# Kernel tuning notes

Hardware: AMD Instinct MI355X
Metric: run time of the kernel (lower is better)

Reference implementation:

```python
import jax, jax.numpy as jnp
import numpy as np

B, C, D, H, W = 2, 32, 96, 96, 96
RED = 16
INV_SQRT2 = 0.7071067811865476  # 1/sqrt(2), Haar analysis filter coefficient
BN_EPS = 1e-5


def _haar1(x, axis):
    # pywt 'haar' DWT on even-length signals: a[i]=(x[2i]+x[2i+1])/sqrt2, d[i]=(x[2i]-x[2i+1])/sqrt2
    e = jax.lax.slice_in_dim(x, 0, None, stride=2, axis=axis)
    o = jax.lax.slice_in_dim(x, 1, None, stride=2, axis=axis)
    return (e + o) * INV_SQRT2, (e - o) * INV_SQRT2


def haar_dwt3d(x):
    # x: (B, C, D, H, W). Separable 3D Haar DWT; key letters follow pywt dwtn
    # axis order (D, H, W): 'aad' = approx along D, approx along H, detail along W.
    aD, dD = _haar1(x, 2)
    aa, ad = _haar1(aD, 3)
    da, dd = _haar1(dD, 3)
    aaa, aad = _haar1(aa, 4)
    ada, add = _haar1(ad, 4)
    daa, dad = _haar1(da, 4)
    dda, ddd = _haar1(dd, 4)
    # per-channel grouping of 7 detail bands, then flatten to (B, 7C, D/2, H/2, W/2)
    high = jnp.stack([aad, ada, add, daa, dad, dda, ddd], axis=2)
    b, c = x.shape[0], x.shape[1]
    high = high.reshape(b, c * 7, *aaa.shape[2:])
    return aaa, high


def chan_attn(x, w1, w2):
    # AdaptiveAvgPool3d(1) -> FC(no bias) -> ReLU -> FC(no bias) -> Sigmoid -> scale
    y = x.mean(axis=(2, 3, 4))                     # (B, Ch)
    y = jax.nn.sigmoid(jnp.maximum(y @ w1.T, 0.0) @ w2.T)
    return x * y[:, :, None, None, None]


def setup_inputs() -> dict:
    key = jax.random.key(0)
    ks = jax.random.split(key, 7)
    x = jax.random.normal(ks[0], (B, C, D, H, W), dtype=jnp.float32)
    w1_low = jax.random.normal(ks[1], (C // RED, C), dtype=jnp.float32) * 0.1
    w2_low = jax.random.normal(ks[2], (C, C // RED), dtype=jnp.float32) * 0.1
    w1_high = jax.random.normal(ks[3], (7 * C // RED, 7 * C), dtype=jnp.float32) * 0.05
    w2_high = jax.random.normal(ks[4], (7 * C, 7 * C // RED), dtype=jnp.float32) * 0.05
    w_fuse = jax.random.normal(ks[5], (C, 8 * C), dtype=jnp.float32) * 0.05  # 1x1x1 conv kernel
    b_fuse = jnp.zeros((C,), dtype=jnp.float32)
    gamma = jnp.ones((C,), dtype=jnp.float32)
    beta = jnp.zeros((C,), dtype=jnp.float32)
    return dict(x=x, w1_low=w1_low, w2_low=w2_low, w1_high=w1_high, w2_high=w2_high,
                w_fuse=w_fuse, b_fuse=b_fuse, gamma=gamma, beta=beta)


def reference(x, w1_low, w2_low, w1_high, w2_high, w_fuse, b_fuse, gamma, beta):
    low, high = haar_dwt3d(x)                                  # (B,C,48,48,48), (B,7C,48,48,48)
    low = chan_attn(low, w1_low, w2_low)
    high = chan_attn(high, w1_high, w2_high)
    z = jnp.concatenate([low, high], axis=1)                   # (B, 8C, 48,48,48)
    z = jnp.einsum('bcdhw,oc->bodhw', z, w_fuse) + b_fuse[None, :, None, None, None]
    # BatchNorm3d (training-mode batch statistics, as fresh torch module defaults)
    mu = z.mean(axis=(0, 2, 3, 4), keepdims=True)
    var = z.var(axis=(0, 2, 3, 4), keepdims=True)
    z = (z - mu) * jax.lax.rsqrt(var + BN_EPS)
    z = z * gamma[None, :, None, None, None] + beta[None, :, None, None, None]
    return jnp.maximum(z, 0.0)
```

## Files before the change

kernel.cpp:

```cpp
#include <hip/hip_runtime.h>
#include <math.h>

#define HS 0.35355339059327373f
#define NSPAT 110592
#define NBN   221184

__global__ __launch_bounds__(256) void k1_parity(const float* __restrict__ x,
                                                 float* __restrict__ S) {
    int blk = blockIdx.x;
    int d   = blk % 96;
    int bc  = blk / 96;
    const float4* x4 = (const float4*)x + (long)blk * 2304;
    int tid = threadIdx.x;
    float aE0 = 0.f, aO0 = 0.f, aE1 = 0.f, aO1 = 0.f;
#pragma unroll
    for (int i = 0; i < 9; ++i) {
        int f = tid + i * 256;
        float4 v = x4[f];
        int h = f / 24;
        float e = v.x + v.z, o = v.y + v.w;
        if (h & 1) { aE1 += e; aO1 += o; }
        else       { aE0 += e; aO0 += o; }
    }
#pragma unroll
    for (int m = 32; m; m >>= 1) {
        aE0 += __shfl_xor(aE0, m, 64); aO0 += __shfl_xor(aO0, m, 64);
        aE1 += __shfl_xor(aE1, m, 64); aO1 += __shfl_xor(aO1, m, 64);
    }
    __shared__ float red[4][4];
    int lane = tid & 63, wave = tid >> 6;
    if (lane == 0) { red[wave][0] = aE0; red[wave][1] = aO0;
                     red[wave][2] = aE1; red[wave][3] = aO1; }
    __syncthreads();
    if (tid < 4) {
        float v = red[0][tid] + red[1][tid] + red[2][tid] + red[3][tid];
        int q = tid >> 1, r = tid & 1, p = d & 1;
        atomicAdd(&S[bc * 8 + p * 4 + q * 2 + r], v);
    }
}

__global__ __launch_bounds__(256) void k2_attn(
        const float* __restrict__ S,
        const float* __restrict__ w1l, const float* __restrict__ w2l,
        const float* __restrict__ w1h, const float* __restrict__ w2h,
        const float* __restrict__ wf, float* __restrict__ A) {
    int b = blockIdx.x, tid = threadIdx.x;
    __shared__ float mlow[32], mhigh[224], h1l[2], h1h[14], ylow[32], yhigh[224];
    const float* Sb = S + b * 256;
    const float MS = HS / (float)NSPAT;
    if (tid < 32) {
        float s = 0.f;
        for (int j = 0; j < 8; ++j) s += Sb[tid * 8 + j];
        mlow[tid] = s * MS;
    }
    if (tid < 224) {
        int c = tid / 7, k = tid % 7, dm = k + 1;
        float s = 0.f;
        for (int j = 0; j < 8; ++j) {
            float sg = (__popc(j & dm) & 1) ? -1.f : 1.f;
            s += sg * Sb[c * 8 + j];
        }
        mhigh[tid] = s * MS;
    }
    __syncthreads();
    if (tid < 2) {
        float s = 0.f;
        for (int c = 0; c < 32; ++c) s += w1l[tid * 32 + c] * mlow[c];
        h1l[tid] = fmaxf(s, 0.f);
    } else if (tid < 16) {
        int j = tid - 2;
        float s = 0.f;
        for (int c = 0; c < 224; ++c) s += w1h[j * 224 + c] * mhigh[c];
        h1h[j] = fmaxf(s, 0.f);
    }
    __syncthreads();
    if (tid < 32) {
        float s = w2l[tid * 2] * h1l[0] + w2l[tid * 2 + 1] * h1l[1];
        ylow[tid] = 1.f / (1.f + expf(-s));
    } else if (tid < 256) {
        int i = tid - 32;
        float s = 0.f;
        for (int j = 0; j < 14; ++j) s += w2h[i * 14 + j] * h1h[j];
        yhigh[i] = 1.f / (1.f + expf(-s));
    }
    __syncthreads();
    for (int idx = tid; idx < 8192; idx += 256) {
        int o = idx >> 8, c = (idx >> 3) & 31, pqr = idx & 7;
        float a = wf[o * 256 + c] * ylow[c];
#pragma unroll
        for (int k = 0; k < 7; ++k) {
            float sg = (__popc(pqr & (k + 1)) & 1) ? -1.f : 1.f;
            a += sg * wf[o * 256 + 32 + c * 7 + k] * yhigh[c * 7 + k];
        }
        A[b * 8192 + idx] = a * HS;
    }
}

__global__ __launch_bounds__(192) void k3_main(const float* __restrict__ x,
                                               const float* __restrict__ A,
                                               float* __restrict__ z,
                                               float* __restrict__ bnSum,
                                               float* __restrict__ bnSq) {
    __shared__ float ldsA[4096];
    __shared__ float red[3][32];
    int blk = blockIdx.x;
    int og  = blk & 1;
    int tmp = blk >> 1;
    int ohg = tmp % 6;
    tmp /= 6;
    int od  = tmp % 48;
    int b   = tmp / 48;
    int tid = threadIdx.x;
    const float* Ab = A + b * 8192 + og * 4096;
    for (int i = tid; i < 4096; i += 192) ldsA[i] = Ab[i];
    __syncthreads();

    int row = tid / 24;
    int t   = tid % 24;
    int oh  = ohg * 8 + row;

    float acc0[16], acc1[16];
#pragma unroll
    for (int o = 0; o < 16; ++o) { acc0[o] = 0.f; acc1[o] = 0.f; }

    const float4* x4 = (const float4*)x;
    int base = (((b * 32) * 96 + 2 * od) * 96 + 2 * oh) * 24 + t;
    for (int c = 0; c < 32; ++c) {
        int i4 = base + c * 221184;
        float4 v00 = x4[i4];
        float4 v01 = x4[i4 + 24];
        float4 v10 = x4[i4 + 2304];
        float4 v11 = x4[i4 + 2304 + 24];
        const float* Ac = &ldsA[c * 8];
#pragma unroll
        for (int o = 0; o < 16; ++o) {
            const float4* Ao = (const float4*)(Ac + o * 256);
            float4 a0 = Ao[0];
            float4 a1 = Ao[1];
            acc0[o] += a0.x * v00.x + a0.y * v00.y + a0.z * v01.x + a0.w * v01.y
                     + a1.x * v10.x + a1.y * v10.y + a1.z * v11.x + a1.w * v11.y;
            acc1[o] += a0.x * v00.z + a0.y * v00.w + a0.z * v01.z + a0.w * v01.w
                     + a1.x * v10.z + a1.y * v10.w + a1.z * v11.z + a1.w * v11.w;
        }
    }

    float2* z2 = (float2*)z;
#pragma unroll
    for (int o = 0; o < 16; ++o) {
        int zi = (((b * 32 + og * 16 + o) * 48 + od) * 48 + oh) * 24 + t;
        z2[zi] = make_float2(acc0[o], acc1[o]);
    }

    int lane = tid & 63, wave = tid >> 6;
#pragma unroll
    for (int o = 0; o < 16; ++o) {
        float sv = acc0[o] + acc1[o];
        float qv = acc0[o] * acc0[o] + acc1[o] * acc1[o];
#pragma unroll
        for (int m = 32; m; m >>= 1) {
            sv += __shfl_xor(sv, m, 64);
            qv += __shfl_xor(qv, m, 64);
        }
        if (lane == 0) { red[wave][o] = sv; red[wave][16 + o] = qv; }
    }
    __syncthreads();
    if (tid < 32) {
        float v = red[0][tid] + red[1][tid] + red[2][tid];
        if (tid < 16) atomicAdd(&bnSum[og * 16 + tid], v);
        else          atomicAdd(&bnSq[og * 16 + tid - 16], v);
    }
}

__global__ __launch_bounds__(256) void k5_norm(float* __restrict__ z,
                                               const float* __restrict__ bnSum,
                                               const float* __restrict__ bnSq,
                                               const float* __restrict__ gamma,
                                               const float* __restrict__ beta) {
    __shared__ float s_sc[32], s_sh[32];
    int tid = threadIdx.x;
    if (tid < 32) {
        const float invN = 1.f / (float)NBN;
        float mean = bnSum[tid] * invN;
        float var  = bnSq[tid] * invN - mean * mean;
        float inv  = rsqrtf(var + 1e-5f);
        float sc   = gamma[tid] * inv;
        s_sc[tid] = sc;
        s_sh[tid] = beta[tid] - mean * sc;
    }
    int i = blockIdx.x * 256 + tid;
    float4* z4 = (float4*)z;
    float4 v = z4[i];
    __syncthreads();
    int o = (i / 27648) & 31;
    float sc = s_sc[o], sh = s_sh[o];
    v.x = fmaxf(v.x * sc + sh, 0.f);
    v.y = fmaxf(v.y * sc + sh, 0.f);
    v.z = fmaxf(v.z * sc + sh, 0.f);
    v.w = fmaxf(v.w * sc + sh, 0.f);
    z4[i] = v;
}

extern "C" void kernel_launch(void* const* d_in, const int* in_sizes, int n_in,
                              void* d_out, int out_size, void* d_ws, size_t ws_size,
                              hipStream_t stream) {
    const float* x    = (const float*)d_in[0];
    const float* w1l  = (const float*)d_in[1];
    const float* w2l  = (const float*)d_in[2];
    const float* w1h  = (const float*)d_in[3];
    const float* w2h  = (const float*)d_in[4];
    const float* wf   = (const float*)d_in[5];
    const float* gamma = (const float*)d_in[7];
    const float* beta  = (const float*)d_in[8];
    float* out = (float*)d_out;

    float* ws    = (float*)d_ws;
    float* S     = ws;
    float* bnSum = ws + 512;
    float* bnSq  = ws + 544;
    float* A     = ws + 1024;

    hipMemsetAsync(d_ws, 0, 576 * sizeof(float), stream);
    k1_parity<<<6144, 256, 0, stream>>>(x, S);
    k2_attn<<<2, 256, 0, stream>>>(S, w1l, w2l, w1h, w2h, wf, A);
    k3_main<<<1152, 192, 0, stream>>>(x, A, out, bnSum, bnSq);
    k5_norm<<<6912, 256, 0, stream>>>(out, bnSum, bnSq, gamma, beta);
}
```

Baseline: 468.8 us.

## Read fuse weights via uniform global loads and prefetch next channel's x

Removes the LDS staging of the 4096-entry fused weight matrix in the main kernel, along with its barrier. Weights are now read directly from global memory at addresses that are uniform across the block, which the compiler can turn into scalar loads. Each iteration also software-prefetches the next input channel's four float4 values so the load overlaps the current channel's FMAs. The cost is more registers, and the risk that scalar loads issued inside the unrolled loop add latency if they are not hoisted.

```diff
diff --git a/kernel.cpp b/kernel.cpp
--- a/kernel.cpp
+++ b/kernel.cpp
@@ -101,7 +101,6 @@
                                                float* __restrict__ z,
                                                float* __restrict__ bnSum,
                                                float* __restrict__ bnSq) {
-    __shared__ float ldsA[4096];
     __shared__ float red[3][32];
     int blk = blockIdx.x;
     int og  = blk & 1;
@@ -111,37 +110,44 @@
     int od  = tmp % 48;
     int b   = tmp / 48;
     int tid = threadIdx.x;
-    const float* Ab = A + b * 8192 + og * 4096;
-    for (int i = tid; i < 4096; i += 192) ldsA[i] = Ab[i];
-    __syncthreads();
-
     int row = tid / 24;
     int t   = tid % 24;
     int oh  = ohg * 8 + row;
 
+    const float* Ab = A + b * 8192 + og * 4096;
+
     float acc0[16], acc1[16];
 #pragma unroll
     for (int o = 0; o < 16; ++o) { acc0[o] = 0.f; acc1[o] = 0.f; }
 
     const float4* x4 = (const float4*)x;
     int base = (((b * 32) * 96 + 2 * od) * 96 + 2 * oh) * 24 + t;
+
+    float4 v00 = x4[base];
+    float4 v01 = x4[base + 24];
+    float4 v10 = x4[base + 2304];
+    float4 v11 = x4[base + 2328];
     for (int c = 0; c < 32; ++c) {
-        int i4 = base + c * 221184;
-        float4 v00 = x4[i4];
-        float4 v01 = x4[i4 + 24];
-        float4 v10 = x4[i4 + 2304];
-        float4 v11 = x4[i4 + 2304 + 24];
-        const float* Ac = &ldsA[c * 8];
+        float4 n00, n01, n10, n11;
+        if (c < 31) {
+            int i4 = base + (c + 1) * 221184;
+            n00 = x4[i4];
+            n01 = x4[i4 + 24];
+            n10 = x4[i4 + 2304];
+            n11 = x4[i4 + 2328];
+        }
+        const float* Ac = Ab + c * 8;
 #pragma unroll
         for (int o = 0; o < 16; ++o) {
-            const float4* Ao = (const float4*)(Ac + o * 256);
-            float4 a0 = Ao[0];
-            float4 a1 = Ao[1];
-            acc0[o] += a0.x * v00.x + a0.y * v00.y + a0.z * v01.x + a0.w * v01.y
-                     + a1.x * v10.x + a1.y * v10.y + a1.z * v11.x + a1.w * v11.y;
-            acc1[o] += a0.x * v00.z + a0.y * v00.w + a0.z * v01.z + a0.w * v01.w
-                     + a1.x * v10.z + a1.y * v10.w + a1.z * v11.z + a1.w * v11.w;
-        }
+            const float* Ao = Ac + o * 256;
+            float a0 = Ao[0], a1 = Ao[1], a2 = Ao[2], a3 = Ao[3];
+            float a4 = Ao[4], a5 = Ao[5], a6 = Ao[6], a7 = Ao[7];
+            acc0[o] += a0 * v00.x + a1 * v00.y + a2 * v01.x + a3 * v01.y
+                     + a4 * v10.x + a5 * v10.y + a6 * v11.x + a7 * v11.y;
+            acc1[o] += a0 * v00.z + a1 * v00.w + a2 * v01.z + a3 * v01.w
+                     + a4 * v10.z + a5 * v10.w + a6 * v11.z + a7 * v11.w;
+        }
+        v00 = n00; v01 = n01; v10 = n10; v11 = n11;
     }
 
     float2* z2 = (float2*)z;
```

After: 441.4 us. 1.06x faster.
